# Kernel optimization log

Hardware: AMD Instinct MI355X
Metric: run time of the kernel (lower is better)

Reference implementation:

```python
import jax, jax.numpy as jnp
import numpy as np

LEVELS = [(64, 64), (32, 32), (16, 16), (8, 8)]  # (H, W) per feature level
B, C, NH, NL, NP, NLAYERS, FFN = 8, 256, 8, 4, 4, 6, 1024
Q = sum(h * w for h, w in LEVELS)  # 5440
DH = C // NH


def setup_inputs() -> dict:
    key = jax.random.key(0)
    ks = iter(jax.random.split(key, 40))
    def rn(shape, s=0.02):
        return jax.random.normal(next(ks), shape, dtype=jnp.float32) * s
    return {
        'src_flat': jax.random.normal(next(ks), (B, Q, C), dtype=jnp.float32),
        'pos_flat': jax.random.normal(next(ks), (B, Q, C), dtype=jnp.float32) * 0.1,
        'level_embed': rn((NL, C), 0.1),
        'W_samp': rn((NLAYERS, C, NH * NL * NP * 2)),
        'b_samp': rn((NLAYERS, NH * NL * NP * 2), 0.1),
        'W_attn': rn((NLAYERS, C, NH * NL * NP)),
        'b_attn': rn((NLAYERS, NH * NL * NP), 0.1),
        'W_val': rn((NLAYERS, C, C)),
        'b_val': jnp.zeros((NLAYERS, C), jnp.float32),
        'W_out': rn((NLAYERS, C, C)),
        'b_out': jnp.zeros((NLAYERS, C), jnp.float32),
        'g1': jnp.ones((NLAYERS, C), jnp.float32),
        'b1': jnp.zeros((NLAYERS, C), jnp.float32),
        'W_fc1': rn((NLAYERS, C, FFN)),
        'b_fc1': jnp.zeros((NLAYERS, FFN), jnp.float32),
        'W_fc2': rn((NLAYERS, FFN, C)),
        'b_fc2': jnp.zeros((NLAYERS, C), jnp.float32),
        'g2': jnp.ones((NLAYERS, C), jnp.float32),
        'b2': jnp.zeros((NLAYERS, C), jnp.float32),
    }


def layer_norm(x, g, b):
    m = x.mean(-1, keepdims=True)
    v = ((x - m) ** 2).mean(-1, keepdims=True)
    return (x - m) * jax.lax.rsqrt(v + 1e-5) * g + b


def get_reference_points():
    # valid_ratios are all ones (masks are all-False), so ref pts are identical per level dim
    pts = []
    for (h, w) in LEVELS:
        ry = (jnp.arange(h, dtype=jnp.float32) + 0.5) / h
        rx = (jnp.arange(w, dtype=jnp.float32) + 0.5) / w
        yy, xx = jnp.meshgrid(ry, rx, indexing='ij')
        pts.append(jnp.stack([xx.ravel(), yy.ravel()], -1))
    return jnp.concatenate(pts, 0)  # [Q, 2] in (x, y)


def ms_deform_attn(query, src, ref_pts, Ws, bs, Wa, ba, Wv, bv, Wo, bo):
    value = (src @ Wv + bv).reshape(B, Q, NH, DH)
    off = (query @ Ws + bs).reshape(B, Q, NH, NL, NP, 2)
    aw = jax.nn.softmax((query @ Wa + ba).reshape(B, Q, NH, NL * NP), axis=-1)
    aw = aw.reshape(B, Q, NH, NL, NP).transpose(0, 2, 1, 3, 4)  # [B,NH,Q,NL,NP]
    normalizer = jnp.array([[w, h] for (h, w) in LEVELS], jnp.float32)  # (x, y) per level
    loc = ref_pts[None, :, None, None, None, :] + off / normalizer[None, None, None, :, None, :]
    out = jnp.zeros((B, NH, Q, DH), jnp.float32)
    start = 0
    for l, (h, w) in enumerate(LEVELS):
        v_l = value[:, start:start + h * w].transpose(0, 2, 1, 3)  # [B,NH,HW,DH]
        start += h * w
        loc_l = loc[:, :, :, l]  # [B,Q,NH,NP,2]
        x = loc_l[..., 0] * w - 0.5  # grid_sample align_corners=False pixel coords
        y = loc_l[..., 1] * h - 0.5
        x0 = jnp.floor(x)
        y0 = jnp.floor(y)
        fx = x - x0
        fy = y - y0
        sampled = jnp.zeros((B, NH, Q, NP, DH), jnp.float32)
        for dy, dx in ((0, 0), (0, 1), (1, 0), (1, 1)):
            cy = y0 + dy
            cx = x0 + dx
            wgt = (fy if dy else 1.0 - fy) * (fx if dx else 1.0 - fx)
            valid = (cy >= 0) & (cy < h) & (cx >= 0) & (cx < w)  # zero padding
            wgt = jnp.where(valid, wgt, 0.0)
            idx = (jnp.clip(cy, 0, h - 1) * w + jnp.clip(cx, 0, w - 1)).astype(jnp.int32)
            idx = idx.transpose(0, 2, 1, 3).reshape(B, NH, Q * NP)
            g = jnp.take_along_axis(v_l, idx[..., None], axis=2).reshape(B, NH, Q, NP, DH)
            sampled = sampled + g * wgt.transpose(0, 2, 1, 3)[..., None]
        out = out + (sampled * aw[:, :, :, l, :, None]).sum(3)
    out = out.transpose(0, 2, 1, 3).reshape(B, Q, C)
    return out @ Wo + bo


def reference(src_flat, pos_flat, level_embed, W_samp, b_samp, W_attn, b_attn, W_val, b_val, W_out, b_out, g1, b1, W_fc1, b_fc1, W_fc2, b_fc2, g2, b2):
    counts = np.array([h * w for h, w in LEVELS])
    lvl_emb = jnp.repeat(level_embed, counts, axis=0, total_repeat_length=Q)  # [Q,C]
    pos = pos_flat + lvl_emb[None]
    ref = get_reference_points()
    out = src_flat
    for i in range(NLAYERS):
        q = out + pos
        attn = ms_deform_attn(q, out, ref, W_samp[i], b_samp[i], W_attn[i], b_attn[i], W_val[i], b_val[i], W_out[i], b_out[i])
        out = layer_norm(out + attn, g1[i], b1[i])
        hid = jax.nn.relu(out @ W_fc1[i] + b_fc1[i]) @ W_fc2[i] + b_fc2[i]
        out = layer_norm(out + hid, g2[i], b2[i])
    return out
```

## Files before the change

kernel.cpp:

```cpp
#include <hip/hip_runtime.h>
#include <hip/hip_bf16.h>

#define NB 8
#define NC 256
#define NH_ 8
#define NLAYERS_ 6
#define FFN_ 1024
#define Q_ 5440
#define DH_ 32
#define M_ (NB*Q_)
#define MC2 (M_/2)

typedef __attribute__((ext_vector_type(8))) short bf16x8;
typedef __attribute__((ext_vector_type(4))) short bf16x4;
typedef __attribute__((ext_vector_type(4))) float f32x4;
typedef __attribute__((ext_vector_type(4))) int i32x4;
typedef __attribute__((ext_vector_type(4))) unsigned int u32x4;
typedef unsigned int u32;

__device__ __forceinline__ unsigned short f2bf(float f) {
  unsigned int u = __float_as_uint(f);
  u += 0x7fffu + ((u >> 16) & 1u);
  return (unsigned short)(u >> 16);
}
__device__ __forceinline__ float bf2f(unsigned short s) {
  return __uint_as_float(((unsigned int)s) << 16);
}
__device__ __forceinline__ void gl16(const unsigned short* g, unsigned short* l) {
  __builtin_amdgcn_global_load_lds((const __attribute__((address_space(1))) u32*)(g),
                                   (__attribute__((address_space(3))) u32*)(l), 16, 0, 0);
}

__global__ void transpose_w2_k(const float* __restrict__ W, unsigned short* __restrict__ Wt,
                               int L, int Kd, int Nd, int NdTot, int nOff) {
  size_t total = (size_t)L * Nd * Kd;
  for (size_t i = (size_t)blockIdx.x * blockDim.x + threadIdx.x; i < total;
       i += (size_t)gridDim.x * blockDim.x) {
    int k = (int)(i % Kd);
    size_t r = i / Kd;
    int n = (int)(r % Nd);
    int l = (int)(r / Nd);
    Wt[((size_t)l * NdTot + nOff + n) * Kd + k] = f2bf(W[((size_t)l * Kd + k) * Nd + n]);
  }
}

__global__ void bias_cat_k(const float* __restrict__ bs, const float* __restrict__ ba,
                           float* __restrict__ bsa) {
  int i = blockIdx.x * blockDim.x + threadIdx.x;
  if (i >= NLAYERS_ * 384) return;
  int l = i / 384, n = i % 384;
  bsa[i] = (n < 256) ? bs[l * 256 + n] : ba[l * 128 + (n - 256)];
}

__global__ __launch_bounds__(256)
void pre_k(const float* __restrict__ src, const float* __restrict__ pf,
           const float* __restrict__ le, unsigned short* __restrict__ xb,
           unsigned short* __restrict__ pe, unsigned short* __restrict__ qb) {
  int row = blockIdx.x * 4 + (threadIdx.x >> 6);
  int lane = threadIdx.x & 63;
  size_t base = (size_t)row * NC + lane * 4;
  int q = row % Q_;
  int lvl = q < 4096 ? 0 : (q < 5120 ? 1 : (q < 5376 ? 2 : 3));
  f32x4 xv = *(const f32x4*)(src + base);
  f32x4 pv = *(const f32x4*)(pf + base) + *(const f32x4*)(le + lvl * NC + lane * 4);
  f32x4 qv = xv + pv;
  bf16x4 xo, po, qo;
#pragma unroll
  for (int j = 0; j < 4; ++j) {
    xo[j] = (short)f2bf(xv[j]); po[j] = (short)f2bf(pv[j]); qo[j] = (short)f2bf(qv[j]);
  }
  *(bf16x4*)(xb + base) = xo;
  *(bf16x4*)(pe + base) = po;
  *(bf16x4*)(qb + base) = qo;
}

__device__ __forceinline__ int swz(int r, int sl) { return sl ^ (r & 3) ^ ((r >> 2) & 3); }
#define ES 136
#define SHN 24576

template <bool RELU>
__device__ __forceinline__ void gemm_body(const unsigned short* X, const unsigned short* Wt,
                                          const float* bias, unsigned short* Y,
                                          int Kdim, int Ndim, int n0, int m0,
                                          unsigned short* SH) {
  const int t = threadIdx.x;
  const int wave = t >> 6, lane = t & 63;
  const int wr = wave >> 1, wc = wave & 1;
  const int lr = lane & 15, lk = lane >> 4;
  const int r0 = t >> 2, sl0 = t & 3;
  const int r1 = (256 + t) >> 2;
  const int gs0 = swz(r0, sl0);
  const int gs1 = swz(r1, sl0);
  const unsigned short* xp0 = X + (size_t)(m0 + r0) * Kdim + gs0 * 8;
  const unsigned short* wp0 = Wt + (size_t)(n0 + r0) * Kdim + gs0 * 8;
  const unsigned short* xp1 = X + (size_t)(m0 + r1) * Kdim + gs1 * 8;
  const unsigned short* wp1 = Wt + (size_t)(n0 + r1) * Kdim + gs1 * 8;

  f32x4 acc[4][4];
#pragma unroll
  for (int i = 0; i < 4; ++i)
#pragma unroll
    for (int j = 0; j < 4; ++j)
#pragma unroll
      for (int e = 0; e < 4; ++e) acc[i][j][e] = 0.f;

  auto stage = [&](int buf, int kt) {
    unsigned short* base = SH + buf * 8192;
    gl16(xp0 + kt, base + t * 8);
    gl16(wp0 + kt, base + 4096 + t * 8);
    gl16(xp1 + kt, base + (256 + t) * 8);
    gl16(wp1 + kt, base + 4096 + (256 + t) * 8);
  };

  const int nt = Kdim >> 5;
  stage(0, 0);
  stage(1, 32);
  asm volatile("s_waitcnt vmcnt(4)" ::: "memory");
  __builtin_amdgcn_s_barrier();

  int buf = 0;
  for (int ti = 0; ti < nt; ++ti) {
    if (ti + 2 < nt) stage(buf == 0 ? 2 : buf - 1, (ti + 2) << 5);
    const unsigned short* Ab = SH + buf * 8192;
    const unsigned short* Bb = Ab + 4096;
    bf16x8 ar[4], br[4];
#pragma unroll
    for (int fi = 0; fi < 4; ++fi) {
      int r = wr * 64 + fi * 16 + lr;
      ar[fi] = *(const bf16x8*)&Ab[r * 32 + swz(r, lk) * 8];
    }
#pragma unroll
    for (int fj = 0; fj < 4; ++fj) {
      int r = wc * 64 + fj * 16 + lr;
      br[fj] = *(const bf16x8*)&Bb[r * 32 + swz(r, lk) * 8];
    }
#pragma unroll
    for (int fi = 0; fi < 4; ++fi)
#pragma unroll
      for (int fj = 0; fj < 4; ++fj)
        acc[fi][fj] = __builtin_amdgcn_mfma_f32_16x16x32_bf16(ar[fi], br[fj], acc[fi][fj], 0, 0, 0);
    if (ti + 2 < nt)
      asm volatile("s_waitcnt vmcnt(4)" ::: "memory");
    else
      asm volatile("s_waitcnt vmcnt(0)" ::: "memory");
    __builtin_amdgcn_s_barrier();
    buf = (buf == 2) ? 0 : buf + 1;
  }

#pragma unroll
  for (int fi = 0; fi < 4; ++fi)
#pragma unroll
    for (int fj = 0; fj < 4; ++fj) {
      int col = wc * 64 + fj * 16 + lr;
      float bv = bias[n0 + col];
#pragma unroll
      for (int rr = 0; rr < 4; ++rr) {
        int row = wr * 64 + fi * 16 + lk * 4 + rr;
        float v = acc[fi][fj][rr] + bv;
        if constexpr (RELU) v = fmaxf(v, 0.f);
        SH[row * ES + col] = f2bf(v);
      }
    }
  __syncthreads();
  {
    int row = t >> 1, hcol = (t & 1) * 64;
    const unsigned short* sp = SH + row * ES + hcol;
    unsigned short* dp = Y + (size_t)(m0 + row) * Ndim + n0 + hcol;
#pragma unroll
    for (int j = 0; j < 8; ++j)
      *(bf16x8*)(dp + j * 8) = *(const bf16x8*)(sp + j * 8);
  }
}

template <bool RELU>
__global__ __launch_bounds__(256)
void gemm_k(const unsigned short* __restrict__ X, const unsigned short* __restrict__ Wt,
            const float* __restrict__ bias, unsigned short* __restrict__ Y,
            int Kdim, int Ndim) {
  __shared__ unsigned short SH[SHN];
  gemm_body<RELU>(X, Wt, bias, Y, Kdim, Ndim, blockIdx.x * 128, blockIdx.y * 128, SH);
}

__global__ __launch_bounds__(256)
void gemm_vs_k(const unsigned short* __restrict__ X0, const unsigned short* __restrict__ W0,
               const float* __restrict__ b0, unsigned short* __restrict__ Y0,
               const unsigned short* __restrict__ X1, const unsigned short* __restrict__ W1,
               const float* __restrict__ b1, unsigned short* __restrict__ Y1) {
  __shared__ unsigned short SH[SHN];
  int bx = blockIdx.x, m0 = blockIdx.y * 128;
  if (bx < 2)
    gemm_body<false>(X0, W0, b0, Y0, 256, 256, bx * 128, m0, SH);
  else
    gemm_body<false>(X1, W1, b1, Y1, 256, 384, (bx - 2) * 128, m0, SH);
}

__global__ __launch_bounds__(256)
void samp_k(const unsigned short* __restrict__ value, const unsigned short* __restrict__ sa,
            unsigned short* __restrict__ attn_feat) {
  __shared__ float lw[4][128][4];
  __shared__ int   la[4][128][4];
  const int wid = threadIdx.x >> 6, lane = threadIdx.x & 63;
  const int bq = blockIdx.x * 4 + wid;
  const int q = bq % Q_;
  const int b = bq / Q_;

  int lvl = q < 4096 ? 0 : (q < 5120 ? 1 : (q < 5376 ? 2 : 3));
  int qrem = q - (lvl == 0 ? 0 : lvl == 1 ? 4096 : lvl == 2 ? 5120 : 5376);
  int wlog = 6 - lvl;
  float inv = __uint_as_float((unsigned)(127 - wlog) << 23);
  float refx = ((qrem & ((1 << wlog) - 1)) + 0.5f) * inv;
  float refy = ((qrem >> wlog) + 0.5f) * inv;
  const unsigned short* sa_bq = sa + (size_t)bq * 384;

  const int h_s = lane >> 3;
  const int s0 = (lane & 7) * 2;
  unsigned lg01 = *(const unsigned*)&sa_bq[256 + h_s * 16 + s0];
  float lg0 = bf2f((unsigned short)(lg01 & 0xffff));
  float lg1 = bf2f((unsigned short)(lg01 >> 16));
  float mx = fmaxf(lg0, lg1);
  mx = fmaxf(mx, __shfl_xor(mx, 1));
  mx = fmaxf(mx, __shfl_xor(mx, 2));
  mx = fmaxf(mx, __shfl_xor(mx, 4));
  float e0 = __expf(lg0 - mx), e1 = __expf(lg1 - mx);
  float sm = e0 + e1;
  sm += __shfl_xor(sm, 1);
  sm += __shfl_xor(sm, 2);
  sm += __shfl_xor(sm, 4);
  float rs = 1.0f / sm;

#pragma unroll
  for (int j = 0; j < 2; ++j) {
    int s = s0 + j;
    float aw = (j ? e1 : e0) * rs;
    unsigned oxy = *(const unsigned*)&sa_bq[h_s * 32 + s * 2];
    float ox = bf2f((unsigned short)(oxy & 0xffff));
    float oy = bf2f((unsigned short)(oxy >> 16));
    int sl = s >> 2;
    int swl = 6 - sl;
    int sw = 1 << swl;
    int sstart = (sl == 0) ? 0 : (sl == 1) ? 4096 : (sl == 2) ? 5120 : 5376;
    float x = fmaf(refx, (float)sw, ox) - 0.5f;
    float y = fmaf(refy, (float)sw, oy) - 0.5f;
    float x0f = floorf(x), y0f = floorf(y);
    float fx = x - x0f, fy = y - y0f;
    int x0 = (int)x0f, y0 = (int)y0f;
    int rowbase = b * Q_ + sstart;
    f32x4 wv; i32x4 av;
#pragma unroll
    for (int c = 0; c < 4; ++c) {
      int dy = c >> 1, dx = c & 1;
      int cy = y0 + dy, cx = x0 + dx;
      float wgt = (dy ? fy : 1.f - fy) * (dx ? fx : 1.f - fx);
      bool valid = (cy >= 0) & (cy < sw) & (cx >= 0) & (cx < sw);
      wgt = valid ? wgt : 0.f;
      int ccy = min(max(cy, 0), sw - 1);
      int ccx = min(max(cx, 0), sw - 1);
      wv[c] = wgt * aw;
      av[c] = ((rowbase + (ccy << swl) + ccx) * NH_ + h_s) * DH_;
    }
    int idx = s * 8 + (h_s ^ (s & 7));
    *(f32x4*)&lw[wid][idx][0] = wv;
    *(i32x4*)&la[wid][idx][0] = av;
  }
  __syncthreads();

  const int h = lane >> 3;
  const int half = (lane >> 2) & 1;
  const int quad = lane & 3;
  const unsigned short* vq = value + quad * 8;
  f32x4 accA = {0.f, 0.f, 0.f, 0.f}, accB = {0.f, 0.f, 0.f, 0.f};
#pragma unroll
  for (int i = 0; i < 8; ++i) {
    int s = half * 8 + i;
    int idx = s * 8 + (h ^ (s & 7));
    f32x4 wv = *(const f32x4*)&lw[wid][idx][0];
    i32x4 av = *(const i32x4*)&la[wid][idx][0];
#pragma unroll
    for (int c = 0; c < 4; ++c) {
      u32x4 g = *(const u32x4*)(vq + av[c]);
      f32x4 v0, v1;
      v0[0] = __uint_as_float(g[0] << 16); v0[1] = __uint_as_float(g[0] & 0xffff0000u);
      v0[2] = __uint_as_float(g[1] << 16); v0[3] = __uint_as_float(g[1] & 0xffff0000u);
      v1[0] = __uint_as_float(g[2] << 16); v1[1] = __uint_as_float(g[2] & 0xffff0000u);
      v1[2] = __uint_as_float(g[3] << 16); v1[3] = __uint_as_float(g[3] & 0xffff0000u);
      float wcc = wv[c];
      accA += v0 * wcc;
      accB += v1 * wcc;
    }
  }
#pragma unroll
  for (int j = 0; j < 4; ++j) {
    accA[j] += __shfl_xor(accA[j], 4);
    accB[j] += __shfl_xor(accB[j], 4);
  }
  if (half == 0) {
    bf16x8 ov;
    ov[0] = (short)f2bf(accA[0]); ov[1] = (short)f2bf(accA[1]);
    ov[2] = (short)f2bf(accA[2]); ov[3] = (short)f2bf(accA[3]);
    ov[4] = (short)f2bf(accB[0]); ov[5] = (short)f2bf(accB[1]);
    ov[6] = (short)f2bf(accB[2]); ov[7] = (short)f2bf(accB[3]);
    *(bf16x8*)(attn_feat + (size_t)bq * NC + h * DH_ + quad * 8) = ov;
  }
}

__device__ __forceinline__ f32x4 ln_core(f32x4 xv, const float* g, const float* bta, int lane) {
  float ssum = xv[0] + xv[1] + xv[2] + xv[3];
#pragma unroll
  for (int o = 1; o <= 32; o <<= 1) ssum += __shfl_xor(ssum, o);
  float mean = ssum * (1.0f / NC);
  f32x4 cv = xv - mean;
  float s2 = cv[0] * cv[0] + cv[1] * cv[1] + cv[2] * cv[2] + cv[3] * cv[3];
#pragma unroll
  for (int o = 1; o <= 32; o <<= 1) s2 += __shfl_xor(s2, o);
  float rstd = rsqrtf(s2 * (1.0f / NC) + 1e-5f);
  f32x4 gv = *(const f32x4*)(g + lane * 4);
  f32x4 bv = *(const f32x4*)(bta + lane * 4);
  return cv * rstd * gv + bv;
}
__device__ __forceinline__ f32x4 ldbf4(const unsigned short* p) {
  bf16x4 v = *(const bf16x4*)p;
  f32x4 r;
#pragma unroll
  for (int j = 0; j < 4; ++j) r[j] = bf2f((unsigned short)v[j]);
  return r;
}
__device__ __forceinline__ void stbf4(unsigned short* p, f32x4 v) {
  bf16x4 o;
#pragma unroll
  for (int j = 0; j < 4; ++j) o[j] = (short)f2bf(v[j]);
  *(bf16x4*)p = o;
}

__global__ __launch_bounds__(256)
void ln_mid_k(const unsigned short* __restrict__ xb, const unsigned short* __restrict__ delta,
              const float* __restrict__ g, const float* __restrict__ bta,
              unsigned short* __restrict__ xm) {
  int row = blockIdx.x * 4 + (threadIdx.x >> 6);
  int lane = threadIdx.x & 63;
  size_t base = (size_t)row * NC + lane * 4;
  f32x4 xv = ldbf4(xb + base) + ldbf4(delta + base);
  f32x4 ov = ln_core(xv, g, bta, lane);
  stbf4(xm + base, ov);
}

template <bool FINAL>
__global__ __launch_bounds__(256)
void ln_end_k(const unsigned short* __restrict__ xm, const unsigned short* __restrict__ delta,
              const float* __restrict__ g, const float* __restrict__ bta,
              const unsigned short* __restrict__ pe,
              unsigned short* __restrict__ xb, unsigned short* __restrict__ qb,
              float* __restrict__ outf) {
  int row = blockIdx.x * 4 + (threadIdx.x >> 6);
  int lane = threadIdx.x & 63;
  size_t base = (size_t)row * NC + lane * 4;
  f32x4 xv = ldbf4(xm + base) + ldbf4(delta + base);
  f32x4 ov = ln_core(xv, g, bta, lane);
  stbf4(xb + base, ov);
  f32x4 qv = ov + ldbf4(pe + base);
  stbf4(qb + base, qv);
  if constexpr (FINAL) *(f32x4*)(outf + base) = ov;
}

extern "C" void kernel_launch(void* const* d_in, const int* in_sizes, int n_in,
                              void* d_out, int out_size, void* d_ws, size_t ws_size,
                              hipStream_t stream) {
  const float* src      = (const float*)d_in[0];
  const float* pos_flat = (const float*)d_in[1];
  const float* lvl_emb  = (const float*)d_in[2];
  const float* W_samp   = (const float*)d_in[3];
  const float* b_samp   = (const float*)d_in[4];
  const float* W_attn   = (const float*)d_in[5];
  const float* b_attn   = (const float*)d_in[6];
  const float* W_val    = (const float*)d_in[7];
  const float* b_val    = (const float*)d_in[8];
  const float* W_out    = (const float*)d_in[9];
  const float* b_out    = (const float*)d_in[10];
  const float* g1       = (const float*)d_in[11];
  const float* b1       = (const float*)d_in[12];
  const float* W_fc1    = (const float*)d_in[13];
  const float* b_fc1    = (const float*)d_in[14];
  const float* W_fc2    = (const float*)d_in[15];
  const float* b_fc2    = (const float*)d_in[16];
  const float* g2       = (const float*)d_in[17];
  const float* b2       = (const float*)d_in[18];

  char* ws = (char*)d_ws;
  size_t o = 0;
  auto alloc = [&](size_t bytes) {
    void* p = ws + o;
    o += (bytes + 255) & ~(size_t)255;
    return p;
  };
  unsigned short* bb    = (unsigned short*)alloc((size_t)MC2 * FFN_ * 2);
  unsigned short* sa    = (unsigned short*)alloc((size_t)M_ * 384 * 2);
  unsigned short* af    = (unsigned short*)alloc((size_t)M_ * NC * 2);
  unsigned short* xb    = (unsigned short*)alloc((size_t)M_ * NC * 2);
  unsigned short* xm    = (unsigned short*)alloc((size_t)M_ * NC * 2);
  unsigned short* qb    = (unsigned short*)alloc((size_t)M_ * NC * 2);
  unsigned short* pe    = (unsigned short*)alloc((size_t)M_ * NC * 2);
  unsigned short* Wv_t  = (unsigned short*)alloc((size_t)6 * 256 * 256 * 2);
  unsigned short* Wsa_t = (unsigned short*)alloc((size_t)6 * 384 * 256 * 2);
  unsigned short* Wo_t  = (unsigned short*)alloc((size_t)6 * 256 * 256 * 2);
  unsigned short* Wf1_t = (unsigned short*)alloc((size_t)6 * 1024 * 256 * 2);
  unsigned short* Wf2_t = (unsigned short*)alloc((size_t)6 * 256 * 1024 * 2);
  float* bsa            = (float*)alloc((size_t)6 * 384 * 4);

  transpose_w2_k<<<1536, 256, 0, stream>>>(W_val, Wv_t, 6, 256, 256, 256, 0);
  transpose_w2_k<<<1536, 256, 0, stream>>>(W_samp, Wsa_t, 6, 256, 256, 384, 0);
  transpose_w2_k<<<768, 256, 0, stream>>>(W_attn, Wsa_t, 6, 256, 128, 384, 256);
  transpose_w2_k<<<1536, 256, 0, stream>>>(W_out, Wo_t, 6, 256, 256, 256, 0);
  transpose_w2_k<<<3072, 256, 0, stream>>>(W_fc1, Wf1_t, 6, 256, 1024, 1024, 0);
  transpose_w2_k<<<3072, 256, 0, stream>>>(W_fc2, Wf2_t, 6, 1024, 256, 256, 0);
  bias_cat_k<<<9, 256, 0, stream>>>(b_samp, b_attn, bsa);
  pre_k<<<M_ / 4, 256, 0, stream>>>(src, pos_flat, lvl_emb, xb, pe, qb);

  for (int i = 0; i < NLAYERS_; ++i) {
    gemm_vs_k<<<dim3(5, M_ / 128), 256, 0, stream>>>(
        xb, Wv_t + (size_t)i * 65536, b_val + i * 256, bb,
        qb, Wsa_t + (size_t)i * 98304, bsa + i * 384, sa);
    samp_k<<<M_ / 4, 256, 0, stream>>>(bb, sa, af);
    gemm_k<false><<<dim3(2, M_ / 128), 256, 0, stream>>>(
        af, Wo_t + (size_t)i * 65536, b_out + i * 256, sa, 256, 256);
    ln_mid_k<<<M_ / 4, 256, 0, stream>>>(xb, sa, g1 + i * 256, b1 + i * 256, xm);
    for (int c = 0; c < 2; ++c) {
      gemm_k<true><<<dim3(8, MC2 / 128), 256, 0, stream>>>(
          xm + (size_t)c * MC2 * NC, Wf1_t + (size_t)i * 262144, b_fc1 + i * 1024, bb, 256, 1024);
      gemm_k<false><<<dim3(2, MC2 / 128), 256, 0, stream>>>(
          bb, Wf2_t + (size_t)i * 262144, b_fc2 + i * 256, sa + (size_t)c * MC2 * NC, 1024, 256);
    }
    if (i == NLAYERS_ - 1)
      ln_end_k<true><<<M_ / 4, 256, 0, stream>>>(xm, sa, g2 + i * 256, b2 + i * 256,
                                                 pe, xb, qb, (float*)d_out);
    else
      ln_end_k<false><<<M_ / 4, 256, 0, stream>>>(xm, sa, g2 + i * 256, b2 + i * 256,
                                                  pe, xb, qb, nullptr);
  }
}
```

Before: 1.660 ms.

## Fuse residual+LayerNorm into full-row 128x256 GEMM epilogues with 512-thread blocks

Adds a 512-thread GEMM kernel with 128x256 output tiles, so each block owns full 256-wide rows. Its epilogue adds the residual and applies LayerNorm, and for the FFN2 GEMM it also writes the query (plus positional embedding) and the final fp32 output. This removes the separate ln_mid and ln_end kernels and their extra passes over the activations. FC1 also moves to 256-wide tiles. The trade-off is fewer blocks for the N=256 GEMMs (one per 128 rows) and a larger LDS footprint.

```diff
diff --git a/kernel.cpp b/kernel.cpp
--- a/kernel.cpp
+++ b/kernel.cpp
@@ -29,6 +29,21 @@
 __device__ __forceinline__ void gl16(const unsigned short* g, unsigned short* l) {
   __builtin_amdgcn_global_load_lds((const __attribute__((address_space(1))) u32*)(g),
                                    (__attribute__((address_space(3))) u32*)(l), 16, 0, 0);
+}
+__device__ __forceinline__ void unp8(bf16x8 v, f32x4& lo, f32x4& hi) {
+  u32x4 g = __builtin_bit_cast(u32x4, v);
+  lo[0] = __uint_as_float(g[0] << 16); lo[1] = __uint_as_float(g[0] & 0xffff0000u);
+  lo[2] = __uint_as_float(g[1] << 16); lo[3] = __uint_as_float(g[1] & 0xffff0000u);
+  hi[0] = __uint_as_float(g[2] << 16); hi[1] = __uint_as_float(g[2] & 0xffff0000u);
+  hi[2] = __uint_as_float(g[3] << 16); hi[3] = __uint_as_float(g[3] & 0xffff0000u);
+}
+__device__ __forceinline__ bf16x8 pck8(f32x4 lo, f32x4 hi) {
+  bf16x8 o;
+  o[0] = (short)f2bf(lo[0]); o[1] = (short)f2bf(lo[1]);
+  o[2] = (short)f2bf(lo[2]); o[3] = (short)f2bf(lo[3]);
+  o[4] = (short)f2bf(hi[0]); o[5] = (short)f2bf(hi[1]);
+  o[6] = (short)f2bf(hi[2]); o[7] = (short)f2bf(hi[3]);
+  return o;
 }
 
 __global__ void transpose_w2_k(const float* __restrict__ W, unsigned short* __restrict__ Wt,
@@ -75,10 +90,10 @@
 }
 
 __device__ __forceinline__ int swz(int r, int sl) { return sl ^ (r & 3) ^ ((r >> 2) & 3); }
+
 #define ES 136
 #define SHN 24576
 
-template <bool RELU>
 __device__ __forceinline__ void gemm_body(const unsigned short* X, const unsigned short* Wt,
                                           const float* bias, unsigned short* Y,
                                           int Kdim, int Ndim, int n0, int m0,
@@ -156,9 +171,7 @@
 #pragma unroll
       for (int rr = 0; rr < 4; ++rr) {
         int row = wr * 64 + fi * 16 + lk * 4 + rr;
-        float v = acc[fi][fj][rr] + bv;
-        if constexpr (RELU) v = fmaxf(v, 0.f);
-        SH[row * ES + col] = f2bf(v);
+        SH[row * ES + col] = f2bf(acc[fi][fj][rr] + bv);
       }
     }
   __syncthreads();
@@ -170,15 +183,6 @@
     for (int j = 0; j < 8; ++j)
       *(bf16x8*)(dp + j * 8) = *(const bf16x8*)(sp + j * 8);
   }
-}
-
-template <bool RELU>
-__global__ __launch_bounds__(256)
-void gemm_k(const unsigned short* __restrict__ X, const unsigned short* __restrict__ Wt,
-            const float* __restrict__ bias, unsigned short* __restrict__ Y,
-            int Kdim, int Ndim) {
-  __shared__ unsigned short SH[SHN];
-  gemm_body<RELU>(X, Wt, bias, Y, Kdim, Ndim, blockIdx.x * 128, blockIdx.y * 128, SH);
 }
 
 __global__ __launch_bounds__(256)
@@ -189,9 +193,172 @@
   __shared__ unsigned short SH[SHN];
   int bx = blockIdx.x, m0 = blockIdx.y * 128;
   if (bx < 2)
-    gemm_body<false>(X0, W0, b0, Y0, 256, 256, bx * 128, m0, SH);
+    gemm_body(X0, W0, b0, Y0, 256, 256, bx * 128, m0, SH);
   else
-    gemm_body<false>(X1, W1, b1, Y1, 256, 384, (bx - 2) * 128, m0, SH);
+    gemm_body(X1, W1, b1, Y1, 256, 384, (bx - 2) * 128, m0, SH);
+}
+
+#define ESW 264
+#define SH512 36864
+
+template <int MODE>
+__global__ __launch_bounds__(512, 4)
+void gemm512_k(const unsigned short* __restrict__ X, const unsigned short* __restrict__ Wt,
+               const float* __restrict__ bias, unsigned short* __restrict__ Y,
+               const unsigned short* __restrict__ res, const float* __restrict__ g,
+               const float* __restrict__ bta, const unsigned short* __restrict__ pe,
+               unsigned short* __restrict__ out1, float* __restrict__ dout,
+               int Kdim, int Ndim, int rowOff) {
+  __shared__ unsigned short SH[SH512];
+  const int t = threadIdx.x;
+  int m0, n0, mOut;
+  if constexpr (MODE == 0) {
+    n0 = (blockIdx.x & 3) * 256;
+    m0 = (blockIdx.x >> 2) * 128;
+    mOut = m0;
+  } else {
+    n0 = 0;
+    m0 = blockIdx.x * 128;
+    mOut = rowOff + m0;
+  }
+  const int wave = t >> 6, lane = t & 63;
+  const int wr = wave >> 2, wc = wave & 3;
+  const int lr = lane & 15, lk = lane >> 4;
+  const int rA = t >> 2, slA = t & 3;
+  const int gsA = swz(rA, slA);
+  const int rB1 = (512 + t) >> 2;
+  const int gsB0 = gsA, gsB1 = swz(rB1, slA);
+  const unsigned short* xp = X + (size_t)(m0 + rA) * Kdim + gsA * 8;
+  const unsigned short* wp0 = Wt + (size_t)(n0 + rA) * Kdim + gsB0 * 8;
+  const unsigned short* wp1 = Wt + (size_t)(n0 + rB1) * Kdim + gsB1 * 8;
+
+  f32x4 acc[4][4];
+#pragma unroll
+  for (int i = 0; i < 4; ++i)
+#pragma unroll
+    for (int j = 0; j < 4; ++j)
+#pragma unroll
+      for (int e = 0; e < 4; ++e) acc[i][j][e] = 0.f;
+
+  auto stage = [&](int buf, int kt) {
+    unsigned short* base = SH + buf * 12288;
+    gl16(xp + kt, base + t * 8);
+    gl16(wp0 + kt, base + 4096 + t * 8);
+    gl16(wp1 + kt, base + 4096 + (512 + t) * 8);
+  };
+
+  const int nt = Kdim >> 5;
+  stage(0, 0);
+  stage(1, 32);
+  asm volatile("s_waitcnt vmcnt(3)" ::: "memory");
+  __builtin_amdgcn_s_barrier();
+
+  int buf = 0;
+  for (int ti = 0; ti < nt; ++ti) {
+    if (ti + 2 < nt) stage(buf == 0 ? 2 : buf - 1, (ti + 2) << 5);
+    const unsigned short* Ab = SH + buf * 12288;
+    const unsigned short* Bb = Ab + 4096;
+    bf16x8 ar[4], br[4];
+#pragma unroll
+    for (int fi = 0; fi < 4; ++fi) {
+      int r = wr * 64 + fi * 16 + lr;
+      ar[fi] = *(const bf16x8*)&Ab[r * 32 + swz(r, lk) * 8];
+    }
+#pragma unroll
+    for (int fj = 0; fj < 4; ++fj) {
+      int r = wc * 64 + fj * 16 + lr;
+      br[fj] = *(const bf16x8*)&Bb[r * 32 + swz(r, lk) * 8];
+    }
+#pragma unroll
+    for (int fi = 0; fi < 4; ++fi)
+#pragma unroll
+      for (int fj = 0; fj < 4; ++fj)
+        acc[fi][fj] = __builtin_amdgcn_mfma_f32_16x16x32_bf16(ar[fi], br[fj], acc[fi][fj], 0, 0, 0);
+    if (ti + 2 < nt)
+      asm volatile("s_waitcnt vmcnt(3)" ::: "memory");
+    else
+      asm volatile("s_waitcnt vmcnt(0)" ::: "memory");
+    __builtin_amdgcn_s_barrier();
+    buf = (buf == 2) ? 0 : buf + 1;
+  }
+
+#pragma unroll
+  for (int fi = 0; fi < 4; ++fi)
+#pragma unroll
+    for (int fj = 0; fj < 4; ++fj) {
+      int col = wc * 64 + fj * 16 + lr;
+      float bv = bias[n0 + col];
+#pragma unroll
+      for (int rr = 0; rr < 4; ++rr) {
+        int row = wr * 64 + fi * 16 + lk * 4 + rr;
+        float v = acc[fi][fj][rr] + bv;
+        if constexpr (MODE == 0) v = fmaxf(v, 0.f);
+        SH[row * ESW + col] = f2bf(v);
+      }
+    }
+  __syncthreads();
+
+  const int row = t >> 2, seg = t & 3;
+  const int c0 = seg * 64;
+  const unsigned short* sp = SH + row * ESW + c0;
+
+  if constexpr (MODE == 0) {
+    unsigned short* dp = Y + (size_t)(mOut + row) * Ndim + n0 + c0;
+#pragma unroll
+    for (int j = 0; j < 8; ++j)
+      *(bf16x8*)(dp + j * 8) = *(const bf16x8*)(sp + j * 8);
+  } else {
+    size_t rbase = (size_t)(mOut + row) * NC + c0;
+    bf16x8 resv[8];
+#pragma unroll
+    for (int j = 0; j < 8; ++j) resv[j] = *(const bf16x8*)(res + rbase + j * 8);
+    float sum = 0.f;
+#pragma unroll
+    for (int j = 0; j < 8; ++j) {
+      f32x4 cl, ch, rl, rh;
+      unp8(*(const bf16x8*)(sp + j * 8), cl, ch);
+      unp8(resv[j], rl, rh);
+      f32x4 a = cl + rl, b = ch + rh;
+      sum += a[0] + a[1] + a[2] + a[3] + b[0] + b[1] + b[2] + b[3];
+    }
+    sum += __shfl_xor(sum, 1);
+    sum += __shfl_xor(sum, 2);
+    float mean = sum * (1.0f / NC);
+    float s2 = 0.f;
+#pragma unroll
+    for (int j = 0; j < 8; ++j) {
+      f32x4 cl, ch, rl, rh;
+      unp8(*(const bf16x8*)(sp + j * 8), cl, ch);
+      unp8(resv[j], rl, rh);
+      f32x4 a = cl + rl - mean, b = ch + rh - mean;
+      s2 += a[0]*a[0] + a[1]*a[1] + a[2]*a[2] + a[3]*a[3]
+          + b[0]*b[0] + b[1]*b[1] + b[2]*b[2] + b[3]*b[3];
+    }
+    s2 += __shfl_xor(s2, 1);
+    s2 += __shfl_xor(s2, 2);
+    float rstd = rsqrtf(s2 * (1.0f / NC) + 1e-5f);
+#pragma unroll
+    for (int j = 0; j < 8; ++j) {
+      int col = c0 + j * 8;
+      f32x4 cl, ch, rl, rh;
+      unp8(*(const bf16x8*)(sp + j * 8), cl, ch);
+      unp8(resv[j], rl, rh);
+      f32x4 gl = *(const f32x4*)(g + col), gh = *(const f32x4*)(g + col + 4);
+      f32x4 bl = *(const f32x4*)(bta + col), bh = *(const f32x4*)(bta + col + 4);
+      f32x4 ol = (cl + rl - mean) * rstd * gl + bl;
+      f32x4 oh = (ch + rh - mean) * rstd * gh + bh;
+      *(bf16x8*)(Y + rbase + j * 8) = pck8(ol, oh);
+      if constexpr (MODE >= 2) {
+        f32x4 pl, ph;
+        unp8(*(const bf16x8*)(pe + rbase + j * 8), pl, ph);
+        *(bf16x8*)(out1 + rbase + j * 8) = pck8(ol + pl, oh + ph);
+      }
+      if constexpr (MODE == 3) {
+        *(f32x4*)(dout + rbase + j * 8) = ol;
+        *(f32x4*)(dout + rbase + j * 8 + 4) = oh;
+      }
+    }
+  }
 }
 
 __global__ __launch_bounds__(256)
@@ -277,12 +444,12 @@
     i32x4 av = *(const i32x4*)&la[wid][idx][0];
 #pragma unroll
     for (int c = 0; c < 4; ++c) {
-      u32x4 g = *(const u32x4*)(vq + av[c]);
+      u32x4 gg = *(const u32x4*)(vq + av[c]);
       f32x4 v0, v1;
-      v0[0] = __uint_as_float(g[0] << 16); v0[1] = __uint_as_float(g[0] & 0xffff0000u);
-      v0[2] = __uint_as_float(g[1] << 16); v0[3] = __uint_as_float(g[1] & 0xffff0000u);
-      v1[0] = __uint_as_float(g[2] << 16); v1[1] = __uint_as_float(g[2] & 0xffff0000u);
-      v1[2] = __uint_as_float(g[3] << 16); v1[3] = __uint_as_float(g[3] & 0xffff0000u);
+      v0[0] = __uint_as_float(gg[0] << 16); v0[1] = __uint_as_float(gg[0] & 0xffff0000u);
+      v0[2] = __uint_as_float(gg[1] << 16); v0[3] = __uint_as_float(gg[1] & 0xffff0000u);
+      v1[0] = __uint_as_float(gg[2] << 16); v1[1] = __uint_as_float(gg[2] & 0xffff0000u);
+      v1[2] = __uint_as_float(gg[3] << 16); v1[3] = __uint_as_float(gg[3] & 0xffff0000u);
       float wcc = wv[c];
       accA += v0 * wcc;
       accB += v1 * wcc;
@@ -294,71 +461,8 @@
     accB[j] += __shfl_xor(accB[j], 4);
   }
   if (half == 0) {
-    bf16x8 ov;
-    ov[0] = (short)f2bf(accA[0]); ov[1] = (short)f2bf(accA[1]);
-    ov[2] = (short)f2bf(accA[2]); ov[3] = (short)f2bf(accA[3]);
-    ov[4] = (short)f2bf(accB[0]); ov[5] = (short)f2bf(accB[1]);
-    ov[6] = (short)f2bf(accB[2]); ov[7] = (short)f2bf(accB[3]);
-    *(bf16x8*)(attn_feat + (size_t)bq * NC + h * DH_ + quad * 8) = ov;
-  }
-}
-
-__device__ __forceinline__ f32x4 ln_core(f32x4 xv, const float* g, const float* bta, int lane) {
-  float ssum = xv[0] + xv[1] + xv[2] + xv[3];
-#pragma unroll
-  for (int o = 1; o <= 32; o <<= 1) ssum += __shfl_xor(ssum, o);
-  float mean = ssum * (1.0f / NC);
-  f32x4 cv = xv - mean;
-  float s2 = cv[0] * cv[0] + cv[1] * cv[1] + cv[2] * cv[2] + cv[3] * cv[3];
-#pragma unroll
-  for (int o = 1; o <= 32; o <<= 1) s2 += __shfl_xor(s2, o);
-  float rstd = rsqrtf(s2 * (1.0f / NC) + 1e-5f);
-  f32x4 gv = *(const f32x4*)(g + lane * 4);
-  f32x4 bv = *(const f32x4*)(bta + lane * 4);
-  return cv * rstd * gv + bv;
-}
-__device__ __forceinline__ f32x4 ldbf4(const unsigned short* p) {
-  bf16x4 v = *(const bf16x4*)p;
-  f32x4 r;
-#pragma unroll
-  for (int j = 0; j < 4; ++j) r[j] = bf2f((unsigned short)v[j]);
-  return r;
-}
-__device__ __forceinline__ void stbf4(unsigned short* p, f32x4 v) {
-  bf16x4 o;
-#pragma unroll
-  for (int j = 0; j < 4; ++j) o[j] = (short)f2bf(v[j]);
-  *(bf16x4*)p = o;
-}
-
-__global__ __launch_bounds__(256)
-void ln_mid_k(const unsigned short* __restrict__ xb, const unsigned short* __restrict__ delta,
-              const float* __restrict__ g, const float* __restrict__ bta,
-              unsigned short* __restrict__ xm) {
-  int row = blockIdx.x * 4 + (threadIdx.x >> 6);
-  int lane = threadIdx.x & 63;
-  size_t base = (size_t)row * NC + lane * 4;
-  f32x4 xv = ldbf4(xb + base) + ldbf4(delta + base);
-  f32x4 ov = ln_core(xv, g, bta, lane);
-  stbf4(xm + base, ov);
-}
-
-template <bool FINAL>
-__global__ __launch_bounds__(256)
-void ln_end_k(const unsigned short* __restrict__ xm, const unsigned short* __restrict__ delta,
-              const float* __restrict__ g, const float* __restrict__ bta,
-              const unsigned short* __restrict__ pe,
-              unsigned short* __restrict__ xb, unsigned short* __restrict__ qb,
-              float* __restrict__ outf) {
-  int row = blockIdx.x * 4 + (threadIdx.x >> 6);
-  int lane = threadIdx.x & 63;
-  size_t base = (size_t)row * NC + lane * 4;
-  f32x4 xv = ldbf4(xm + base) + ldbf4(delta + base);
-  f32x4 ov = ln_core(xv, g, bta, lane);
-  stbf4(xb + base, ov);
-  f32x4 qv = ov + ldbf4(pe + base);
-  stbf4(qb + base, qv);
-  if constexpr (FINAL) *(f32x4*)(outf + base) = ov;
+    *(bf16x8*)(attn_feat + (size_t)bq * NC + h * DH_ + quad * 8) = pck8(accA, accB);
+  }
 }
 
 extern "C" void kernel_launch(void* const* d_in, const int* in_sizes, int n_in,
@@ -419,20 +523,22 @@
         xb, Wv_t + (size_t)i * 65536, b_val + i * 256, bb,
         qb, Wsa_t + (size_t)i * 98304, bsa + i * 384, sa);
     samp_k<<<M_ / 4, 256, 0, stream>>>(bb, sa, af);
-    gemm_k<false><<<dim3(2, M_ / 128), 256, 0, stream>>>(
-        af, Wo_t + (size_t)i * 65536, b_out + i * 256, sa, 256, 256);
-    ln_mid_k<<<M_ / 4, 256, 0, stream>>>(xb, sa, g1 + i * 256, b1 + i * 256, xm);
+    gemm512_k<1><<<M_ / 128, 512, 0, stream>>>(
+        af, Wo_t + (size_t)i * 65536, b_out + i * 256, xm,
+        xb, g1 + i * 256, b1 + i * 256, nullptr, nullptr, nullptr, 256, 256, 0);
     for (int c = 0; c < 2; ++c) {
-      gemm_k<true><<<dim3(8, MC2 / 128), 256, 0, stream>>>(
-          xm + (size_t)c * MC2 * NC, Wf1_t + (size_t)i * 262144, b_fc1 + i * 1024, bb, 256, 1024);
-      gemm_k<false><<<dim3(2, MC2 / 128), 256, 0, stream>>>(
-          bb, Wf2_t + (size_t)i * 262144, b_fc2 + i * 256, sa + (size_t)c * MC2 * NC, 1024, 256);
-    }
-    if (i == NLAYERS_ - 1)
-      ln_end_k<true><<<M_ / 4, 256, 0, stream>>>(xm, sa, g2 + i * 256, b2 + i * 256,
-                                                 pe, xb, qb, (float*)d_out);
-    else
-      ln_end_k<false><<<M_ / 4, 256, 0, stream>>>(xm, sa, g2 + i * 256, b2 + i * 256,
-                                                  pe, xb, qb, nullptr);
-  }
-}
+      int rowOff = c * MC2;
+      gemm512_k<0><<<(MC2 / 128) * 4, 512, 0, stream>>>(
+          xm + (size_t)rowOff * NC, Wf1_t + (size_t)i * 262144, b_fc1 + i * 1024, bb,
+          nullptr, nullptr, nullptr, nullptr, nullptr, nullptr, 256, 1024, 0);
+      if (i == NLAYERS_ - 1)
+        gemm512_k<3><<<MC2 / 128, 512, 0, stream>>>(
+            bb, Wf2_t + (size_t)i * 262144, b_fc2 + i * 256, xb,
+            xm, g2 + i * 256, b2 + i * 256, pe, qb, (float*)d_out, 1024, 256, rowOff);
+      else
+        gemm512_k<2><<<MC2 / 128, 512, 0, stream>>>(
+            bb, Wf2_t + (size_t)i * 262144, b_fc2 + i * 256, xb,
+            xm, g2 + i * 256, b2 + i * 256, pe, qb, nullptr, 1024, 256, rowOff);
+    }
+  }
+}
```

Measured after the change: 1.778 ms. 7.1% more time.
